# Performance work log

Measured on AMD Instinct MI355X. Metric: run time of the kernel, lower is better.

## Reference

```python
import jax, jax.numpy as jnp
import numpy as np

FACTOR = 0.25  # lossFunc(factor=0.25)


def _argmax_coords(x):
    # x: [B, H, W] -> [B, 2] float coords (row, col) of the max element.
    # Matches (p == p.max()).nonzero().float() when the max is unique
    # (true a.s. for continuous random inputs).
    B, H, W = x.shape
    idx = jnp.argmax(x.reshape(B, H * W), axis=-1)
    return jnp.stack([idx // W, idx % W], axis=-1).astype(x.dtype)


def setup_inputs() -> dict:
    key = jax.random.key(0)
    k1, k2 = jax.random.split(key)
    pred = jax.random.normal(k1, (64, 512, 512), dtype=jnp.float32)
    label = jax.random.normal(k2, (64, 1, 512, 512), dtype=jnp.float32)
    return {"pred": pred, "label": label}


def reference(pred, label):
    label0 = label[:, 0]                      # [B, H, W]
    B = pred.shape[0]
    # Vectorized replacement of the per-sample Python loop:
    cp = _argmax_coords(pred)                 # [B, 2]
    cl = _argmax_coords(label0)               # [B, 2]
    # sum-reduced MSE over coordinates (size_average=False), summed over batch
    idx_loss = jnp.sum((cp - cl) ** 2)
    # sum-reduced MSE over all elements
    mse_loss = jnp.sum((pred - label0) ** 2)
    # alpha comes from .item() in torch -> a constant scalar
    alpha = jnp.where(idx_loss != 0, mse_loss / idx_loss, jnp.asarray(1.0, pred.dtype))
    alpha = jax.lax.stop_gradient(alpha)
    loss = (mse_loss + FACTOR * alpha * idx_loss) / B
    return loss
```

## Files before the change

### kernel.cpp

```cpp
#include <hip/hip_runtime.h>
#include <math.h>

#define HW 262144
#define BPB 64
#define CHUNK 4096

__device__ __forceinline__ unsigned int fmono(float f) {
    unsigned int u = __float_as_uint(f);
    return (u & 0x80000000u) ? ~u : (u | 0x80000000u);
}

__global__ __launch_bounds__(256) void reduce_kernel(
    const float* __restrict__ pred, const float* __restrict__ label,
    unsigned long long* __restrict__ pp, unsigned long long* __restrict__ lp,
    float* __restrict__ mse)
{
    const int bi = blockIdx.x;
    const int b = bi >> 6;
    const int chunk = bi & (BPB - 1);
    const float4* p4 = (const float4*)(pred + (size_t)b * HW) + (size_t)chunk * (CHUNK / 4);
    const float4* l4 = (const float4*)(label + (size_t)b * HW) + (size_t)chunk * (CHUNK / 4);
    const int t = threadIdx.x;
    const unsigned int base = (unsigned int)chunk * CHUNK;

    float4 P[4], L[4];
#pragma unroll
    for (int i = 0; i < 4; ++i) {
        P[i] = p4[i * 256 + t];
        L[i] = l4[i * 256 + t];
    }

    float sumsq = 0.0f;
    float pmax = -INFINITY, lmax = -INFINITY;
    unsigned int pidx = 0, lidx = 0;

#pragma unroll
    for (int i = 0; i < 4; ++i) {
        const float4 p = P[i];
        const float4 l = L[i];
        const unsigned int e = base + ((unsigned int)(i * 256 + t)) * 4;
        float d;
        d = p.x - l.x; sumsq += d * d;
        d = p.y - l.y; sumsq += d * d;
        d = p.z - l.z; sumsq += d * d;
        d = p.w - l.w; sumsq += d * d;
        if (p.x > pmax) { pmax = p.x; pidx = e;     }
        if (p.y > pmax) { pmax = p.y; pidx = e + 1; }
        if (p.z > pmax) { pmax = p.z; pidx = e + 2; }
        if (p.w > pmax) { pmax = p.w; pidx = e + 3; }
        if (l.x > lmax) { lmax = l.x; lidx = e;     }
        if (l.y > lmax) { lmax = l.y; lidx = e + 1; }
        if (l.z > lmax) { lmax = l.z; lidx = e + 2; }
        if (l.w > lmax) { lmax = l.w; lidx = e + 3; }
    }

    unsigned long long ppk = ((unsigned long long)fmono(pmax) << 32) | (unsigned long long)(0xFFFFFFFFu - pidx);
    unsigned long long lpk = ((unsigned long long)fmono(lmax) << 32) | (unsigned long long)(0xFFFFFFFFu - lidx);

    for (int off = 32; off > 0; off >>= 1) {
        sumsq += __shfl_down(sumsq, off);
        unsigned long long o;
        o = __shfl_down(ppk, off); if (o > ppk) ppk = o;
        o = __shfl_down(lpk, off); if (o > lpk) lpk = o;
    }

    __shared__ float s_sum[4];
    __shared__ unsigned long long s_pp[4], s_lp[4];
    const int wave = t >> 6, lane = t & 63;
    if (lane == 0) { s_sum[wave] = sumsq; s_pp[wave] = ppk; s_lp[wave] = lpk; }
    __syncthreads();
    if (t == 0) {
        float s = s_sum[0] + s_sum[1] + s_sum[2] + s_sum[3];
        unsigned long long P2 = s_pp[0], L2 = s_lp[0];
        #pragma unroll
        for (int i = 1; i < 4; ++i) {
            if (s_pp[i] > P2) P2 = s_pp[i];
            if (s_lp[i] > L2) L2 = s_lp[i];
        }
        atomicAdd(mse, s);
        atomicMax(&pp[b], P2);
        atomicMax(&lp[b], L2);
    }
}

__global__ void finalize_kernel(const unsigned long long* __restrict__ pp,
                                const unsigned long long* __restrict__ lp,
                                const float* __restrict__ mse,
                                float* __restrict__ out)
{
    const int i = threadIdx.x;
    const unsigned int ip = 0xFFFFFFFFu - (unsigned int)(pp[i] & 0xFFFFFFFFull);
    const unsigned int il = 0xFFFFFFFFu - (unsigned int)(lp[i] & 0xFFFFFFFFull);
    const float rp = (float)(ip >> 9), cp = (float)(ip & 511u);
    const float rl = (float)(il >> 9), cl = (float)(il & 511u);
    float d = (rp - rl) * (rp - rl) + (cp - cl) * (cp - cl);
    for (int off = 32; off > 0; off >>= 1) d += __shfl_down(d, off);
    if (i == 0) {
        const float m = *mse;
        const float alpha = (d != 0.0f) ? (m / d) : 1.0f;
        out[0] = (m + 0.25f * alpha * d) / 64.0f;
    }
}

extern "C" void kernel_launch(void* const* d_in, const int* in_sizes, int n_in,
                              void* d_out, int out_size, void* d_ws, size_t ws_size,
                              hipStream_t stream) {
    const float* pred  = (const float*)d_in[0];
    const float* label = (const float*)d_in[1];
    float* out = (float*)d_out;

    unsigned long long* pp = (unsigned long long*)d_ws;
    unsigned long long* lp = pp + 64;
    float* mse = (float*)(lp + 64);

    hipMemsetAsync(d_ws, 0, 2 * 64 * sizeof(unsigned long long) + sizeof(float), stream);

    reduce_kernel<<<dim3(64 * BPB), dim3(256), 0, stream>>>(pred, label, pp, lp, mse);
    finalize_kernel<<<dim3(1), dim3(64), 0, stream>>>(pp, lp, mse, out);
}
```

Baseline: 169.0 us.

## Replace global atomics with per-block partials and drop workspace memset

Each block now processes 8192 elements with 8 float4 loads per tensor issued up front, and a scheduling barrier keeps the loads grouped. Per-block partial max keys and sums are written to the workspace instead of being combined with global atomics. A 1024-thread finalize kernel reduces all partials, so the memset launch is no longer needed. The aim is to remove atomic contention and one launch while keeping more loads in flight. The cost is higher register pressure per thread and fewer blocks overall.

```diff
diff --git a/kernel.cpp b/kernel.cpp
--- a/kernel.cpp
+++ b/kernel.cpp
@@ -2,8 +2,9 @@
 #include <math.h>
 
 #define HW 262144
-#define BPB 64
-#define CHUNK 4096
+#define BPB 32
+#define CHUNK 8192
+#define NBLK (64 * BPB)
 
 __device__ __forceinline__ unsigned int fmono(float f) {
     unsigned int u = __float_as_uint(f);
@@ -12,30 +13,30 @@
 
 __global__ __launch_bounds__(256) void reduce_kernel(
     const float* __restrict__ pred, const float* __restrict__ label,
-    unsigned long long* __restrict__ pp, unsigned long long* __restrict__ lp,
-    float* __restrict__ mse)
+    unsigned long long* __restrict__ pblk, unsigned long long* __restrict__ lblk,
+    float* __restrict__ sblk)
 {
     const int bi = blockIdx.x;
-    const int b = bi >> 6;
+    const int b = bi >> 5;
     const int chunk = bi & (BPB - 1);
     const float4* p4 = (const float4*)(pred + (size_t)b * HW) + (size_t)chunk * (CHUNK / 4);
     const float4* l4 = (const float4*)(label + (size_t)b * HW) + (size_t)chunk * (CHUNK / 4);
     const int t = threadIdx.x;
     const unsigned int base = (unsigned int)chunk * CHUNK;
 
-    float4 P[4], L[4];
+    float4 P[8], L[8];
 #pragma unroll
-    for (int i = 0; i < 4; ++i) {
-        P[i] = p4[i * 256 + t];
-        L[i] = l4[i * 256 + t];
-    }
+    for (int i = 0; i < 8; ++i) P[i] = p4[i * 256 + t];
+#pragma unroll
+    for (int i = 0; i < 8; ++i) L[i] = l4[i * 256 + t];
+    __builtin_amdgcn_sched_barrier(0);
 
     float sumsq = 0.0f;
     float pmax = -INFINITY, lmax = -INFINITY;
     unsigned int pidx = 0, lidx = 0;
 
 #pragma unroll
-    for (int i = 0; i < 4; ++i) {
+    for (int i = 0; i < 8; ++i) {
         const float4 p = P[i];
         const float4 l = L[i];
         const unsigned int e = base + ((unsigned int)(i * 256 + t)) * 4;
@@ -72,33 +73,61 @@
     if (t == 0) {
         float s = s_sum[0] + s_sum[1] + s_sum[2] + s_sum[3];
         unsigned long long P2 = s_pp[0], L2 = s_lp[0];
-        #pragma unroll
+#pragma unroll
         for (int i = 1; i < 4; ++i) {
             if (s_pp[i] > P2) P2 = s_pp[i];
             if (s_lp[i] > L2) L2 = s_lp[i];
         }
-        atomicAdd(mse, s);
-        atomicMax(&pp[b], P2);
-        atomicMax(&lp[b], L2);
+        pblk[bi] = P2;
+        lblk[bi] = L2;
+        sblk[bi] = s;
     }
 }
 
-__global__ void finalize_kernel(const unsigned long long* __restrict__ pp,
-                                const unsigned long long* __restrict__ lp,
-                                const float* __restrict__ mse,
-                                float* __restrict__ out)
+__global__ __launch_bounds__(1024) void finalize_kernel(
+    const unsigned long long* __restrict__ pblk,
+    const unsigned long long* __restrict__ lblk,
+    const float* __restrict__ sblk,
+    float* __restrict__ out)
 {
-    const int i = threadIdx.x;
-    const unsigned int ip = 0xFFFFFFFFu - (unsigned int)(pp[i] & 0xFFFFFFFFull);
-    const unsigned int il = 0xFFFFFFFFu - (unsigned int)(lp[i] & 0xFFFFFFFFull);
-    const float rp = (float)(ip >> 9), cp = (float)(ip & 511u);
-    const float rl = (float)(il >> 9), cl = (float)(il & 511u);
-    float d = (rp - rl) * (rp - rl) + (cp - cl) * (cp - cl);
-    for (int off = 32; off > 0; off >>= 1) d += __shfl_down(d, off);
-    if (i == 0) {
-        const float m = *mse;
-        const float alpha = (d != 0.0f) ? (m / d) : 1.0f;
-        out[0] = (m + 0.25f * alpha * d) / 64.0f;
+    const int t = threadIdx.x;
+
+    float s = sblk[t] + sblk[t + 1024];
+    for (int off = 32; off > 0; off >>= 1) s += __shfl_down(s, off);
+    __shared__ float ss[16];
+    const int wave = t >> 6;
+    if ((t & 63) == 0) ss[wave] = s;
+
+    const int batch = t >> 4, j = t & 15;
+    unsigned long long Pv = pblk[batch * 32 + j];
+    unsigned long long o  = pblk[batch * 32 + j + 16];
+    if (o > Pv) Pv = o;
+    unsigned long long Lv = lblk[batch * 32 + j];
+    o = lblk[batch * 32 + j + 16];
+    if (o > Lv) Lv = o;
+    for (int off = 8; off > 0; off >>= 1) {
+        o = __shfl_down(Pv, off, 16); if (o > Pv) Pv = o;
+        o = __shfl_down(Lv, off, 16); if (o > Lv) Lv = o;
+    }
+    __shared__ float dd[64];
+    if (j == 0) {
+        const unsigned int ip = 0xFFFFFFFFu - (unsigned int)(Pv & 0xFFFFFFFFull);
+        const unsigned int il = 0xFFFFFFFFu - (unsigned int)(Lv & 0xFFFFFFFFull);
+        const float rp = (float)(ip >> 9), cp = (float)(ip & 511u);
+        const float rl = (float)(il >> 9), cl = (float)(il & 511u);
+        dd[batch] = (rp - rl) * (rp - rl) + (cp - cl) * (cp - cl);
+    }
+    __syncthreads();
+    if (t < 64) {
+        float d = dd[t];
+        for (int off = 32; off > 0; off >>= 1) d += __shfl_down(d, off);
+        if (t == 0) {
+            float m = 0.0f;
+#pragma unroll
+            for (int i = 0; i < 16; ++i) m += ss[i];
+            const float alpha = (d != 0.0f) ? (m / d) : 1.0f;
+            out[0] = (m + 0.25f * alpha * d) / 64.0f;
+        }
     }
 }
 
@@ -109,12 +138,10 @@
     const float* label = (const float*)d_in[1];
     float* out = (float*)d_out;
 
-    unsigned long long* pp = (unsigned long long*)d_ws;
-    unsigned long long* lp = pp + 64;
-    float* mse = (float*)(lp + 64);
+    unsigned long long* pblk = (unsigned long long*)d_ws;
+    unsigned long long* lblk = pblk + NBLK;
+    float* sblk = (float*)(lblk + NBLK);
 
-    hipMemsetAsync(d_ws, 0, 2 * 64 * sizeof(unsigned long long) + sizeof(float), stream);
-
-    reduce_kernel<<<dim3(64 * BPB), dim3(256), 0, stream>>>(pred, label, pp, lp, mse);
-    finalize_kernel<<<dim3(1), dim3(64), 0, stream>>>(pp, lp, mse, out);
+    reduce_kernel<<<dim3(NBLK), dim3(256), 0, stream>>>(pred, label, pblk, lblk, sblk);
+    finalize_kernel<<<dim3(1), dim3(1024), 0, stream>>>(pblk, lblk, sblk, out);
 }
```

Result: faster. 143.2 us (-15.3%).
